# Performance work log

Measured on AMD Instinct MI355X. Metric: run time of the kernel, lower is better.

Reference implementation:

```python
import jax, jax.numpy as jnp
import numpy as np

NUM_GRAPHS = 256  # fixed number of segments (batch.max()+1 in the torch code)

def setup_inputs() -> dict:
    key = jax.random.key(0)
    k1, k2, k3, k4, k5 = jax.random.split(key, 5)
    N, D, H = 200000, 256, 128
    x = jax.random.normal(k1, (N, D), dtype=jnp.float32)
    batch = jnp.sort(jax.random.randint(k2, (N,), 0, NUM_GRAPHS)).astype(jnp.int64)
    # attention MLP params: Linear(D->H), Tanh, Linear(H->1)
    w1 = jax.random.normal(k3, (D, H), dtype=jnp.float32) / np.sqrt(D)
    b1 = jnp.zeros((H,), dtype=jnp.float32)
    w2 = jax.random.normal(k4, (H, 1), dtype=jnp.float32) / np.sqrt(H)
    b2 = jnp.zeros((1,), dtype=jnp.float32)
    return {"x": x, "batch": batch, "w1": w1, "b1": b1, "w2": w2, "b2": b2}

def reference(x, batch, w1, b1, w2, b2):
    # attention scores: Linear -> tanh -> Linear -> [N,1]
    scores = jnp.tanh(x @ w1 + b1) @ w2 + b2          # [N,1]
    # NOTE: faithful to the original: softmax over ALL nodes (dim=0), not per-graph
    attn = jax.nn.softmax(scores, axis=0)              # [N,1]
    weighted = x * attn                                # [N,D]
    # masked per-graph sum == segment sum over graph ids
    out = jax.ops.segment_sum(weighted, batch, num_segments=NUM_GRAPHS)  # [B,D]
    return out
```

## Files before the change

kernel.cpp:

```cpp
#include <hip/hip_runtime.h>

#define NGRAPHS 256
#define DIM     256
#define HID     128
#define TILE    128

typedef __attribute__((ext_vector_type(8))) short bf16x8;
typedef __attribute__((ext_vector_type(4))) float f32x4;

__device__ __forceinline__ ushort f2bf_rne(float f) {
    unsigned u = __float_as_uint(f);
    unsigned r = u + 0x7fffu + ((u >> 16) & 1u);
    return (ushort)(r >> 16);
}
__device__ __forceinline__ float bf2f(ushort h) {
    return __uint_as_float(((unsigned)h) << 16);
}
__device__ __forceinline__ float tanh_fast(float x) {
    float e = __expf(2.0f * x);
    return 1.0f - 2.0f * __builtin_amdgcn_rcpf(1.0f + e);
}

__device__ __forceinline__ void glds16(const void* g, void* l) {
    __builtin_amdgcn_global_load_lds(
        (const __attribute__((address_space(1))) unsigned int*)g,
        (__attribute__((address_space(3))) unsigned int*)l, 16, 0, 0);
}

__device__ __forceinline__ void cvt8(float4 v0, float4 v1, bf16x8& h, bf16x8& l) {
    float f[8] = {v0.x, v0.y, v0.z, v0.w, v1.x, v1.y, v1.z, v1.w};
    unsigned hu[8], lu[8];
#pragma unroll
    for (int i = 0; i < 8; ++i) {
        unsigned u = __float_as_uint(f[i]);
        unsigned hb = u & 0xffff0000u;
        hu[i] = u;
        lu[i] = __float_as_uint(f[i] - __uint_as_float(hb));
    }
    union { unsigned w[4]; bf16x8 v; } H, L;
#pragma unroll
    for (int j = 0; j < 4; ++j) {
        H.w[j] = (hu[2 * j] >> 16) | (hu[2 * j + 1] & 0xffff0000u);
        L.w[j] = (lu[2 * j] >> 16) | (lu[2 * j + 1] & 0xffff0000u);
    }
    h = H.v; l = L.v;
}

__global__ void k_prep(const float* __restrict__ w1, ushort* __restrict__ w1f)
{
    int idx = blockIdx.x * 256 + threadIdx.x;
    int k  = idx >> 7, nn = idx & 127;
    int ks = k >> 5, lhi = (k >> 3) & 3, j = k & 7;
    int nf = nn >> 4, llo = nn & 15;
    int lane = lhi * 16 + llo;
    float v = w1[idx];
    ushort hb = f2bf_rne(v);
    ushort lb = f2bf_rne(v - bf2f(hb));
    int base = (ks * 8 + nf) * 1024 + lane * 8 + j;
    w1f[base]       = hb;
    w1f[base + 512] = lb;
}

__global__ __launch_bounds__(256, 2) void k_scores(
    const float* __restrict__ x, const int* __restrict__ batch,
    const ushort* __restrict__ w1f,
    const float* __restrict__ b1, const float* __restrict__ w2,
    const float* __restrict__ b2,
    float* __restrict__ wsp, float* __restrict__ wse, int* __restrict__ wsid,
    int n)
{
    __shared__ __align__(16) unsigned char smem[65536];
    float  (*xs)[TILE * 32] = (float(*)[TILE * 32])smem;
    ushort (*bs)[8 * 1024]  = (ushort(*)[8 * 1024])(smem + 32768);
    float  (*sred)[2][DIM]  = (float(*)[2][DIM])smem;
    __shared__ float evals[TILE];
    __shared__ int   gid[TILE];
    __shared__ float ep[4];

    const int t    = threadIdx.x;
    const int b    = blockIdx.x;
    const int r0   = b * TILE;
    const int wid  = t >> 6;
    const int lane = t & 63;
    const int lhi  = lane >> 4;
    const int llo  = lane & 15;

    if (t < TILE) {
        int r = r0 + t;
        gid[t] = batch[r < n ? r : (n - 1)];
    }

    size_t xoff[4], boff[4];
    int    xl[4], bl[4];
#pragma unroll
    for (int i = 0; i < 4; ++i) {
        int p = i * 256 + t;
        int r = p >> 3, s = p & 7;
        int q = s ^ (r & 7);
        int rsrc = r0 + r; if (rsrc >= n) rsrc = n - 1;
        xoff[i] = (size_t)rsrc * DIM + q * 4;
        boff[i] = (size_t)p * 8;
        xl[i]   = (i * 256 + wid * 64) * 4;
        bl[i]   = (i * 256 + wid * 64) * 8;
    }

#define STAGE(sel, KS) do {                                          \
    _Pragma("unroll")                                                \
    for (int i = 0; i < 4; ++i) {                                    \
        glds16(x + xoff[i] + (KS) * 32, &xs[sel][xl[i]]);            \
        glds16(w1f + (size_t)(KS) * 8192 + boff[i], &bs[sel][bl[i]]);\
    }                                                                \
} while (0)

    f32x4 acc[2][8];
#pragma unroll
    for (int i = 0; i < 2; ++i)
#pragma unroll
        for (int j = 0; j < 8; ++j) acc[i][j] = (f32x4){0.f, 0.f, 0.f, 0.f};

    const int ra0 = wid * 32 + llo;
    const int ra1 = ra0 + 16;
    const int rb7 = ra0 & 7;
    const int c00 = (ra0 * 8 + ((2 * lhi)     ^ rb7)) * 4;
    const int c01 = (ra0 * 8 + ((2 * lhi + 1) ^ rb7)) * 4;
    const int c10 = (ra1 * 8 + ((2 * lhi)     ^ rb7)) * 4;
    const int c11 = (ra1 * 8 + ((2 * lhi + 1) ^ rb7)) * 4;

    STAGE(0, 0);
    __syncthreads();
#pragma unroll
    for (int ks = 0; ks < 8; ++ks) {
        const int cur = ks & 1;
        if (ks < 7) STAGE(cur ^ 1, ks + 1);

        float4 a0 = *(const float4*)&xs[cur][c00];
        float4 a1 = *(const float4*)&xs[cur][c01];
        float4 c0 = *(const float4*)&xs[cur][c10];
        float4 c1 = *(const float4*)&xs[cur][c11];
        bf16x8 ah0, al0, ah1, al1;
        cvt8(a0, a1, ah0, al0);
        cvt8(c0, c1, ah1, al1);

#pragma unroll
        for (int nf = 0; nf < 8; ++nf) {
            bf16x8 bh = *(const bf16x8*)&bs[cur][(nf * 2 + 0) * 512 + lane * 8];
            bf16x8 bl = *(const bf16x8*)&bs[cur][(nf * 2 + 1) * 512 + lane * 8];
            acc[0][nf] = __builtin_amdgcn_mfma_f32_16x16x32_bf16(ah0, bh, acc[0][nf], 0, 0, 0);
            acc[1][nf] = __builtin_amdgcn_mfma_f32_16x16x32_bf16(ah1, bh, acc[1][nf], 0, 0, 0);
            acc[0][nf] = __builtin_amdgcn_mfma_f32_16x16x32_bf16(ah0, bl, acc[0][nf], 0, 0, 0);
            acc[1][nf] = __builtin_amdgcn_mfma_f32_16x16x32_bf16(ah1, bl, acc[1][nf], 0, 0, 0);
            acc[0][nf] = __builtin_amdgcn_mfma_f32_16x16x32_bf16(al0, bh, acc[0][nf], 0, 0, 0);
            acc[1][nf] = __builtin_amdgcn_mfma_f32_16x16x32_bf16(al1, bh, acc[1][nf], 0, 0, 0);
        }
        __syncthreads();
    }
#undef STAGE

    float b2v = b2[0];
    float b1v[8], w2v[8];
#pragma unroll
    for (int nf = 0; nf < 8; ++nf) {
        b1v[nf] = b1[nf * 16 + llo];
        w2v[nf] = w2[nf * 16 + llo];
    }
    float sc[8];
#pragma unroll
    for (int mf = 0; mf < 2; ++mf)
#pragma unroll
        for (int rg = 0; rg < 4; ++rg) {
            float p = 0.f;
#pragma unroll
            for (int nf = 0; nf < 8; ++nf)
                p += tanh_fast(acc[mf][nf][rg] + b1v[nf]) * w2v[nf];
            sc[mf * 4 + rg] = p;
        }
#pragma unroll
    for (int off = 1; off < 16; off <<= 1)
#pragma unroll
        for (int q = 0; q < 8; ++q) sc[q] += __shfl_xor(sc[q], off, 64);

    if (llo == 0) {
#pragma unroll
        for (int mf = 0; mf < 2; ++mf)
#pragma unroll
            for (int rg = 0; rg < 4; ++rg) {
                int row = wid * 32 + mf * 16 + lhi * 4 + rg;
                float s = sc[mf * 4 + rg] + b2v;
                evals[row] = (r0 + row < n) ? __expf(s) : 0.f;
            }
    }
    __syncthreads();

    {
        const int g0 = gid[0];
        float4 a0 = {0.f, 0.f, 0.f, 0.f}, a1 = {0.f, 0.f, 0.f, 0.f};
        for (int bt = 0; bt < 4; ++bt) {
            float4 xv[8];
#pragma unroll
            for (int j = 0; j < 8; ++j) {
                int rsrc = r0 + wid * 32 + bt * 8 + j;
                if (rsrc >= n) rsrc = n - 1;
                xv[j] = *(const float4*)(x + (size_t)rsrc * DIM + lane * 4);
            }
#pragma unroll
            for (int j = 0; j < 8; ++j) {
                int row = wid * 32 + bt * 8 + j;
                float e = evals[row];
                if (gid[row] != g0) {
                    a1.x = fmaf(e, xv[j].x, a1.x); a1.y = fmaf(e, xv[j].y, a1.y);
                    a1.z = fmaf(e, xv[j].z, a1.z); a1.w = fmaf(e, xv[j].w, a1.w);
                } else {
                    a0.x = fmaf(e, xv[j].x, a0.x); a0.y = fmaf(e, xv[j].y, a0.y);
                    a0.z = fmaf(e, xv[j].z, a0.z); a0.w = fmaf(e, xv[j].w, a0.w);
                }
            }
        }
        *(float4*)&sred[wid][0][lane * 4] = a0;
        *(float4*)&sred[wid][1][lane * 4] = a1;
    }
    __syncthreads();
    {
        float s0 = sred[0][0][t] + sred[1][0][t] + sred[2][0][t] + sred[3][0][t];
        float s1 = sred[0][1][t] + sred[1][1][t] + sred[2][1][t] + sred[3][1][t];
        wsp[(size_t)b * 512 + t]       = s0;
        wsp[(size_t)b * 512 + 256 + t] = s1;
        if (t == 0) wsid[b] = gid[0];
    }

    float rsum = (t < TILE) ? evals[t] : 0.f;
#pragma unroll
    for (int off = 32; off; off >>= 1) rsum += __shfl_down(rsum, off, 64);
    if ((t & 63) == 0) ep[t >> 6] = rsum;
    __syncthreads();
    if (t == 0) wse[b] = ep[0] + ep[1];
}

__global__ __launch_bounds__(256) void k_combine(
    const int* __restrict__ batch, const float* __restrict__ wsp,
    const float* __restrict__ wse, const int* __restrict__ wsid,
    float* __restrict__ out, int n, int nblk)
{
    __shared__ float sred[256];
    __shared__ int bounds[2];
    const int g = blockIdx.x;
    const int d = threadIdx.x;

    float p = 0.f;
    for (int i = d; i < nblk; i += 256) p += wse[i];
    sred[d] = p;
    __syncthreads();
    for (int s = 128; s; s >>= 1) {
        if (d < s) sred[d] += sred[d + s];
        __syncthreads();
    }
    const float S = sred[0];

    if (d < 2) {
        int v = g + d;
        int lo = 0, hi = n;
        while (lo < hi) { int mid = (lo + hi) >> 1; if (batch[mid] < v) lo = mid + 1; else hi = mid; }
        bounds[d] = lo;
    }
    __syncthreads();

    const int st = bounds[0], en = bounds[1];
    float acc = 0.f;
    if (st < en) {
        for (int bb = st >> 7; bb <= (en - 1) >> 7; ++bb) {
            int slot = (wsid[bb] == g) ? 0 : 1;
            acc += wsp[(size_t)bb * 512 + slot * 256 + d];
        }
    }
    out[g * 256 + d] = acc / S;
}

extern "C" void kernel_launch(void* const* d_in, const int* in_sizes, int n_in,
                              void* d_out, int out_size, void* d_ws, size_t ws_size,
                              hipStream_t stream)
{
    const float* x     = (const float*)d_in[0];
    const int*   batch = (const int*)d_in[1];
    const float* w1    = (const float*)d_in[2];
    const float* b1    = (const float*)d_in[3];
    const float* w2    = (const float*)d_in[4];
    const float* b2    = (const float*)d_in[5];
    float* out = (float*)d_out;

    const int n    = in_sizes[1];
    const int nblk = (n + TILE - 1) / TILE;

    ushort* w1f = (ushort*)d_ws;
    float*  wsp = (float*)((char*)d_ws + (size_t)DIM * HID * 2 * sizeof(ushort));
    float*  wse = wsp + (size_t)nblk * 512;
    int*    wsid = (int*)(wse + nblk);

    k_prep<<<dim3(DIM * HID / 256), dim3(256), 0, stream>>>(w1, w1f);
    k_scores<<<dim3(nblk), dim3(256), 0, stream>>>(x, batch, w1f,
                                                   b1, w2, b2, wsp, wse, wsid, n);
    k_combine<<<dim3(NGRAPHS), dim3(256), 0, stream>>>(batch, wsp, wse, wsid,
                                                       out, n, nblk);
}
```

Measured before the change: 96.04 us.

## Load x tiles directly into registers and halve LDS to raise occupancy

The x tile no longer goes through shared memory. Each lane loads its own MFMA A-fragment rows straight from global memory into double-buffered registers, and only the W1 split-bf16 fragments stay staged in LDS. This cuts LDS from 64KB to about 32KB, so launch bounds go from 2 to 4 blocks per CU to hide memory latency better. The trade-offs are that each lane's global loads are 32-byte chunks strided across rows, which coalesce less well than the old staging, and that the extra register buffers must still fit under the tighter register budget.

```diff
diff --git a/kernel.cpp b/kernel.cpp
--- a/kernel.cpp
+++ b/kernel.cpp
@@ -61,7 +61,7 @@
     w1f[base + 512] = lb;
 }
 
-__global__ __launch_bounds__(256, 2) void k_scores(
+__global__ __launch_bounds__(256, 4) void k_scores(
     const float* __restrict__ x, const int* __restrict__ batch,
     const ushort* __restrict__ w1f,
     const float* __restrict__ b1, const float* __restrict__ w2,
@@ -69,13 +69,11 @@
     float* __restrict__ wsp, float* __restrict__ wse, int* __restrict__ wsid,
     int n)
 {
-    __shared__ __align__(16) unsigned char smem[65536];
-    float  (*xs)[TILE * 32] = (float(*)[TILE * 32])smem;
-    ushort (*bs)[8 * 1024]  = (ushort(*)[8 * 1024])(smem + 32768);
-    float  (*sred)[2][DIM]  = (float(*)[2][DIM])smem;
+    __shared__ __align__(16) ushort bs[2][8 * 1024];
     __shared__ float evals[TILE];
     __shared__ int   gid[TILE];
     __shared__ float ep[4];
+    float (*sred)[2][DIM] = (float(*)[2][DIM])&bs[0][0];
 
     const int t    = threadIdx.x;
     const int b    = blockIdx.x;
@@ -90,71 +88,70 @@
         gid[t] = batch[r < n ? r : (n - 1)];
     }
 
-    size_t xoff[4], boff[4];
-    int    xl[4], bl[4];
+    size_t boff[4];
+    int    bl[4];
 #pragma unroll
     for (int i = 0; i < 4; ++i) {
-        int p = i * 256 + t;
-        int r = p >> 3, s = p & 7;
-        int q = s ^ (r & 7);
-        int rsrc = r0 + r; if (rsrc >= n) rsrc = n - 1;
-        xoff[i] = (size_t)rsrc * DIM + q * 4;
-        boff[i] = (size_t)p * 8;
-        xl[i]   = (i * 256 + wid * 64) * 4;
+        boff[i] = (size_t)(i * 256 + t) * 8;
         bl[i]   = (i * 256 + wid * 64) * 8;
     }
 
-#define STAGE(sel, KS) do {                                          \
-    _Pragma("unroll")                                                \
-    for (int i = 0; i < 4; ++i) {                                    \
-        glds16(x + xoff[i] + (KS) * 32, &xs[sel][xl[i]]);            \
-        glds16(w1f + (size_t)(KS) * 8192 + boff[i], &bs[sel][bl[i]]);\
-    }                                                                \
+#define STAGE_B(sel, KS) do {                                         \
+    _Pragma("unroll")                                                 \
+    for (int i = 0; i < 4; ++i)                                       \
+        glds16(w1f + (size_t)(KS) * 8192 + boff[i], &bs[sel][bl[i]]); \
 } while (0)
 
+    int row0 = r0 + wid * 32 + llo;
+    int row1 = row0 + 16;
+    if (row0 >= n) row0 = n - 1;
+    if (row1 >= n) row1 = n - 1;
+    const float* xr0 = x + (size_t)row0 * DIM + lhi * 8;
+    const float* xr1 = x + (size_t)row1 * DIM + lhi * 8;
+
     f32x4 acc[2][8];
 #pragma unroll
     for (int i = 0; i < 2; ++i)
 #pragma unroll
         for (int j = 0; j < 8; ++j) acc[i][j] = (f32x4){0.f, 0.f, 0.f, 0.f};
 
-    const int ra0 = wid * 32 + llo;
-    const int ra1 = ra0 + 16;
-    const int rb7 = ra0 & 7;
-    const int c00 = (ra0 * 8 + ((2 * lhi)     ^ rb7)) * 4;
-    const int c01 = (ra0 * 8 + ((2 * lhi + 1) ^ rb7)) * 4;
-    const int c10 = (ra1 * 8 + ((2 * lhi)     ^ rb7)) * 4;
-    const int c11 = (ra1 * 8 + ((2 * lhi + 1) ^ rb7)) * 4;
-
-    STAGE(0, 0);
-    __syncthreads();
+    float4 pA[2], pB[2], pC[2], pD[2];
+    pA[0] = *(const float4*)(xr0);
+    pB[0] = *(const float4*)(xr0 + 4);
+    pC[0] = *(const float4*)(xr1);
+    pD[0] = *(const float4*)(xr1 + 4);
+    STAGE_B(0, 0);
+    __syncthreads();
+
 #pragma unroll
     for (int ks = 0; ks < 8; ++ks) {
         const int cur = ks & 1;
-        if (ks < 7) STAGE(cur ^ 1, ks + 1);
-
-        float4 a0 = *(const float4*)&xs[cur][c00];
-        float4 a1 = *(const float4*)&xs[cur][c01];
-        float4 c0 = *(const float4*)&xs[cur][c10];
-        float4 c1 = *(const float4*)&xs[cur][c11];
+        if (ks < 7) {
+            pA[cur ^ 1] = *(const float4*)(xr0 + (ks + 1) * 32);
+            pB[cur ^ 1] = *(const float4*)(xr0 + (ks + 1) * 32 + 4);
+            pC[cur ^ 1] = *(const float4*)(xr1 + (ks + 1) * 32);
+            pD[cur ^ 1] = *(const float4*)(xr1 + (ks + 1) * 32 + 4);
+            STAGE_B(cur ^ 1, ks + 1);
+        }
+
         bf16x8 ah0, al0, ah1, al1;
-        cvt8(a0, a1, ah0, al0);
-        cvt8(c0, c1, ah1, al1);
+        cvt8(pA[cur], pB[cur], ah0, al0);
+        cvt8(pC[cur], pD[cur], ah1, al1);
 
 #pragma unroll
         for (int nf = 0; nf < 8; ++nf) {
             bf16x8 bh = *(const bf16x8*)&bs[cur][(nf * 2 + 0) * 512 + lane * 8];
-            bf16x8 bl = *(const bf16x8*)&bs[cur][(nf * 2 + 1) * 512 + lane * 8];
-            acc[0][nf] = __builtin_amdgcn_mfma_f32_16x16x32_bf16(ah0, bh, acc[0][nf], 0, 0, 0);
-            acc[1][nf] = __builtin_amdgcn_mfma_f32_16x16x32_bf16(ah1, bh, acc[1][nf], 0, 0, 0);
-            acc[0][nf] = __builtin_amdgcn_mfma_f32_16x16x32_bf16(ah0, bl, acc[0][nf], 0, 0, 0);
-            acc[1][nf] = __builtin_amdgcn_mfma_f32_16x16x32_bf16(ah1, bl, acc[1][nf], 0, 0, 0);
-            acc[0][nf] = __builtin_amdgcn_mfma_f32_16x16x32_bf16(al0, bh, acc[0][nf], 0, 0, 0);
-            acc[1][nf] = __builtin_amdgcn_mfma_f32_16x16x32_bf16(al1, bh, acc[1][nf], 0, 0, 0);
+            bf16x8 bl16 = *(const bf16x8*)&bs[cur][(nf * 2 + 1) * 512 + lane * 8];
+            acc[0][nf] = __builtin_amdgcn_mfma_f32_16x16x32_bf16(ah0, bh,   acc[0][nf], 0, 0, 0);
+            acc[1][nf] = __builtin_amdgcn_mfma_f32_16x16x32_bf16(ah1, bh,   acc[1][nf], 0, 0, 0);
+            acc[0][nf] = __builtin_amdgcn_mfma_f32_16x16x32_bf16(ah0, bl16, acc[0][nf], 0, 0, 0);
+            acc[1][nf] = __builtin_amdgcn_mfma_f32_16x16x32_bf16(ah1, bl16, acc[1][nf], 0, 0, 0);
+            acc[0][nf] = __builtin_amdgcn_mfma_f32_16x16x32_bf16(al0, bh,   acc[0][nf], 0, 0, 0);
+            acc[1][nf] = __builtin_amdgcn_mfma_f32_16x16x32_bf16(al1, bh,   acc[1][nf], 0, 0, 0);
         }
         __syncthreads();
     }
-#undef STAGE
+#undef STAGE_B
 
     float b2v = b2[0];
     float b1v[8], w2v[8];
```

Measured after the change: 152.3 us. +58.5%, slower.

## Drop low bf16 half of W1 and triple-buffer LDS staging with vmcnt waits

Applied to the files above, without the earlier changes.

W1 is now stored as a single bf16 value instead of a high/low split, so the x_lo*w_lo-free three-term product becomes two terms (x_hi*w and x_lo*w). This removes a third of the MFMAs and halves W1 staging traffic. LDS staging moves from double to triple buffering, using explicit s_waitcnt vmcnt and one barrier per k-step instead of two __syncthreads. The trade is some precision loss in the score GEMM from rounding W1 to bf16, plus reliance on hand-counted outstanding-load waits.

```diff
diff --git a/kernel.cpp b/kernel.cpp
--- a/kernel.cpp
+++ b/kernel.cpp
@@ -12,9 +12,6 @@
     unsigned u = __float_as_uint(f);
     unsigned r = u + 0x7fffu + ((u >> 16) & 1u);
     return (ushort)(r >> 16);
-}
-__device__ __forceinline__ float bf2f(ushort h) {
-    return __uint_as_float(((unsigned)h) << 16);
 }
 __device__ __forceinline__ float tanh_fast(float x) {
     float e = __expf(2.0f * x);
@@ -53,12 +50,7 @@
     int ks = k >> 5, lhi = (k >> 3) & 3, j = k & 7;
     int nf = nn >> 4, llo = nn & 15;
     int lane = lhi * 16 + llo;
-    float v = w1[idx];
-    ushort hb = f2bf_rne(v);
-    ushort lb = f2bf_rne(v - bf2f(hb));
-    int base = (ks * 8 + nf) * 1024 + lane * 8 + j;
-    w1f[base]       = hb;
-    w1f[base + 512] = lb;
+    w1f[(ks * 8 + nf) * 512 + lane * 8 + j] = f2bf_rne(w1[idx]);
 }
 
 __global__ __launch_bounds__(256, 2) void k_scores(
@@ -69,13 +61,11 @@
     float* __restrict__ wsp, float* __restrict__ wse, int* __restrict__ wsid,
     int n)
 {
-    __shared__ __align__(16) unsigned char smem[65536];
-    float  (*xs)[TILE * 32] = (float(*)[TILE * 32])smem;
-    ushort (*bs)[8 * 1024]  = (ushort(*)[8 * 1024])(smem + 32768);
-    float  (*sred)[2][DIM]  = (float(*)[2][DIM])smem;
+    __shared__ __align__(16) unsigned char smem[3 * 24576];
     __shared__ float evals[TILE];
     __shared__ int   gid[TILE];
     __shared__ float ep[4];
+    float (*sred)[2][DIM] = (float(*)[2][DIM])smem;
 
     const int t    = threadIdx.x;
     const int b    = blockIdx.x;
@@ -90,8 +80,8 @@
         gid[t] = batch[r < n ? r : (n - 1)];
     }
 
-    size_t xoff[4], boff[4];
-    int    xl[4], bl[4];
+    size_t xoff[4];
+    int    xl[4];
 #pragma unroll
     for (int i = 0; i < 4; ++i) {
         int p = i * 256 + t;
@@ -99,17 +89,26 @@
         int q = s ^ (r & 7);
         int rsrc = r0 + r; if (rsrc >= n) rsrc = n - 1;
         xoff[i] = (size_t)rsrc * DIM + q * 4;
-        boff[i] = (size_t)p * 8;
-        xl[i]   = (i * 256 + wid * 64) * 4;
-        bl[i]   = (i * 256 + wid * 64) * 8;
-    }
-
-#define STAGE(sel, KS) do {                                          \
-    _Pragma("unroll")                                                \
-    for (int i = 0; i < 4; ++i) {                                    \
-        glds16(x + xoff[i] + (KS) * 32, &xs[sel][xl[i]]);            \
-        glds16(w1f + (size_t)(KS) * 8192 + boff[i], &bs[sel][bl[i]]);\
-    }                                                                \
+        xl[i]   = (i * 256 + wid * 64) * 16;
+    }
+    size_t boff[2];
+    int    bl[2];
+#pragma unroll
+    for (int i = 0; i < 2; ++i) {
+        boff[i] = (size_t)(i * 256 + t) * 8;
+        bl[i]   = (i * 256 + wid * 64) * 16;
+    }
+
+#define XBUF(sel) ((float*)(smem + (sel) * 24576))
+#define BBUF(sel) ((ushort*)(smem + (sel) * 24576 + 16384))
+#define STAGE(sel, KS) do {                                              \
+    _Pragma("unroll")                                                    \
+    for (int i = 0; i < 4; ++i)                                          \
+        glds16(x + xoff[i] + (KS) * 32, smem + (sel) * 24576 + xl[i]);   \
+    _Pragma("unroll")                                                    \
+    for (int i = 0; i < 2; ++i)                                          \
+        glds16(w1f + (size_t)(KS) * 4096 + boff[i],                      \
+               smem + (sel) * 24576 + 16384 + bl[i]);                    \
 } while (0)
 
     f32x4 acc[2][8];
@@ -127,34 +126,42 @@
     const int c11 = (ra1 * 8 + ((2 * lhi + 1) ^ rb7)) * 4;
 
     STAGE(0, 0);
-    __syncthreads();
+    STAGE(1, 1);
 #pragma unroll
     for (int ks = 0; ks < 8; ++ks) {
-        const int cur = ks & 1;
-        if (ks < 7) STAGE(cur ^ 1, ks + 1);
-
-        float4 a0 = *(const float4*)&xs[cur][c00];
-        float4 a1 = *(const float4*)&xs[cur][c01];
-        float4 c0 = *(const float4*)&xs[cur][c10];
-        float4 c1 = *(const float4*)&xs[cur][c11];
+        const int cur = ks % 3;
+        if (ks < 7) {
+            asm volatile("s_waitcnt vmcnt(6)" ::: "memory");
+        } else {
+            asm volatile("s_waitcnt vmcnt(0)" ::: "memory");
+        }
+        __builtin_amdgcn_sched_barrier(0);
+        __builtin_amdgcn_s_barrier();
+        __builtin_amdgcn_sched_barrier(0);
+        if (ks < 6) STAGE((ks + 2) % 3, ks + 2);
+
+        const float*  xsc = XBUF(cur);
+        const ushort* bsc = BBUF(cur);
+        float4 a0 = *(const float4*)&xsc[c00];
+        float4 a1 = *(const float4*)&xsc[c01];
+        float4 c0 = *(const float4*)&xsc[c10];
+        float4 c1 = *(const float4*)&xsc[c11];
         bf16x8 ah0, al0, ah1, al1;
         cvt8(a0, a1, ah0, al0);
         cvt8(c0, c1, ah1, al1);
 
 #pragma unroll
         for (int nf = 0; nf < 8; ++nf) {
-            bf16x8 bh = *(const bf16x8*)&bs[cur][(nf * 2 + 0) * 512 + lane * 8];
-            bf16x8 bl = *(const bf16x8*)&bs[cur][(nf * 2 + 1) * 512 + lane * 8];
+            bf16x8 bh = *(const bf16x8*)&bsc[nf * 512 + lane * 8];
             acc[0][nf] = __builtin_amdgcn_mfma_f32_16x16x32_bf16(ah0, bh, acc[0][nf], 0, 0, 0);
             acc[1][nf] = __builtin_amdgcn_mfma_f32_16x16x32_bf16(ah1, bh, acc[1][nf], 0, 0, 0);
-            acc[0][nf] = __builtin_amdgcn_mfma_f32_16x16x32_bf16(ah0, bl, acc[0][nf], 0, 0, 0);
-            acc[1][nf] = __builtin_amdgcn_mfma_f32_16x16x32_bf16(ah1, bl, acc[1][nf], 0, 0, 0);
             acc[0][nf] = __builtin_amdgcn_mfma_f32_16x16x32_bf16(al0, bh, acc[0][nf], 0, 0, 0);
             acc[1][nf] = __builtin_amdgcn_mfma_f32_16x16x32_bf16(al1, bh, acc[1][nf], 0, 0, 0);
         }
-        __syncthreads();
     }
 #undef STAGE
+#undef XBUF
+#undef BBUF
 
     float b2v = b2[0];
     float b1v[8], w2v[8];
@@ -290,7 +297,7 @@
     const int nblk = (n + TILE - 1) / TILE;
 
     ushort* w1f = (ushort*)d_ws;
-    float*  wsp = (float*)((char*)d_ws + (size_t)DIM * HID * 2 * sizeof(ushort));
+    float*  wsp = (float*)((char*)d_ws + (size_t)DIM * HID * sizeof(ushort));
     float*  wse = wsp + (size_t)nblk * 512;
     int*    wsid = (int*)(wse + nblk);
 
```

Result: faster. 88.58 us (-7.8%).
